# Optimization experiments

Measured on AMD Instinct MI355X. Metric: run time of the kernel, lower is better.

Reference implementation:

```python
import jax, jax.numpy as jnp
import numpy as np

EPS = 1e-5
GROUPS = 8


def _gn_per_channel(x, w, b):
    # GroupNorm with num_groups == num_channels: per-channel instance norm over (h, w)
    m = x.mean(axis=(2, 3), keepdims=True)
    v = x.var(axis=(2, 3), keepdims=True)  # biased var, matches torch GroupNorm
    xn = (x - m) * jax.lax.rsqrt(v + EPS)
    return xn * w[None, :, None, None] + b[None, :, None, None]


def setup_inputs() -> dict:
    key = jax.random.key(0)
    k0, k1 = jax.random.split(key)
    b, c, h, w = 16, 512, 64, 64
    cg = c // GROUPS          # 64 per-group channels
    half = cg // 2            # 32
    x = jax.random.normal(k0, (b, c, h, w), jnp.float32)
    conv1x1_w = jax.random.normal(k1, (cg, cg), jnp.float32) / np.float32(np.sqrt(cg))
    conv1x1_b = jnp.zeros((cg,), jnp.float32)
    gn_w = jnp.ones((cg,), jnp.float32)
    gn_b = jnp.zeros((cg,), jnp.float32)
    gn1_w = jnp.ones((half,), jnp.float32)
    gn1_b = jnp.zeros((half,), jnp.float32)
    cweight = jnp.zeros((1, half, 1, 1), jnp.float32)
    cbias = jnp.ones((1, half, 1, 1), jnp.float32)
    sweight = jnp.zeros((1, half, 1, 1), jnp.float32)
    sbias = jnp.ones((1, half, 1, 1), jnp.float32)
    return {"x": x, "conv1x1_w": conv1x1_w, "conv1x1_b": conv1x1_b,
            "gn_w": gn_w, "gn_b": gn_b, "gn1_w": gn1_w, "gn1_b": gn1_b,
            "cweight": cweight, "cbias": cbias, "sweight": sweight, "sbias": sbias}


def reference(x, conv1x1_w, conv1x1_b, gn_w, gn_b, gn1_w, gn1_b,
              cweight, cbias, sweight, sbias):
    b, c, h, w = x.shape
    g = GROUPS
    cg = c // g
    half = cg // 2
    bg = b * g
    gx = x.reshape(bg, cg, h, w)  # group_x

    # coordinate-attention branch: pool along W and H
    x_h = gx.mean(axis=3, keepdims=True)                      # (bg, cg, h, 1)
    x_w = gx.mean(axis=2, keepdims=True).transpose(0, 1, 3, 2)  # (bg, cg, w, 1)
    hw_cat = jnp.concatenate([x_h, x_w], axis=2)              # (bg, cg, h+w, 1)
    hw = jnp.einsum('oi,bilk->bolk', conv1x1_w, hw_cat) + conv1x1_b[None, :, None, None]
    xh = hw[:, :, :h]                       # (bg, cg, h, 1)
    xw = hw[:, :, h:].transpose(0, 1, 3, 2)  # (bg, cg, 1, w)
    x1 = _gn_per_channel(gx * jax.nn.sigmoid(xh) * jax.nn.sigmoid(xw), gn_w, gn_b)

    # shuffle-attention branch on chunked channels
    x0, x1b = gx[:, :half], gx[:, half:]
    xc = x0.mean(axis=(2, 3), keepdims=True)                  # (bg, half, 1, 1)
    x_channel = x0 * jax.nn.sigmoid(cweight * xc + cbias)
    xs = _gn_per_channel(x1b, gn1_w, gn1_b)
    x_spatial = x1b * jax.nn.sigmoid(sweight * xs + sbias)
    out = jnp.concatenate([x_channel, x_spatial], axis=1)     # (bg, cg, h, w)
    # channel shuffle with g=2
    x2 = out.reshape(bg, 2, half, h, w).transpose(0, 2, 1, 3, 4).reshape(bg, cg, h, w)

    # cross-branch attention weights via small batched matmuls
    x11 = jax.nn.softmax(x1.mean(axis=(2, 3)).reshape(bg, 1, cg), axis=-1)
    x21 = jax.nn.softmax(x2.mean(axis=(2, 3)).reshape(bg, 1, cg), axis=-1)
    x12 = x2.reshape(bg, cg, h * w)
    x22 = x1.reshape(bg, cg, h * w)
    weights = (jnp.matmul(x11, x12) + jnp.matmul(x21, x22)).reshape(bg, 1, h, w)
    return (gx * jax.nn.sigmoid(weights)).reshape(b, c, h, w)
```

## Files before the change

kernel.cpp:

```cpp
#include <hip/hip_runtime.h>
#include <math.h>

#define EPSV 1e-5f

__device__ __forceinline__ float fast_rcp(float x) {
#if __has_builtin(__builtin_amdgcn_rcpf)
    return __builtin_amdgcn_rcpf(x);
#else
    return 1.0f / x;
#endif
}

__device__ __forceinline__ float sigmoidf_(float x) {
    return fast_rcp(1.0f + __expf(-x));
}

__global__ __launch_bounds__(256) void k_stats1(
    const float* __restrict__ x,
    float* __restrict__ rowmean,
    float* __restrict__ colmean,
    float* __restrict__ meanA,
    float* __restrict__ varA)
{
    int blk = blockIdx.x;
    const float4* p4 = (const float4*)(x + (size_t)blk * 4096);
    int t = threadIdx.x;
    int g = t >> 4, cl = t & 15;
    float cp0 = 0.f, cp1 = 0.f, cp2 = 0.f, cp3 = 0.f, s = 0.f, ss = 0.f;
    __shared__ float colacc[16][64];
    __shared__ float red[8];
#pragma unroll
    for (int k = 0; k < 4; ++k) {
        float4 v = p4[t + 256 * k];
        float rp = v.x + v.y + v.z + v.w;
        s += rp;
        ss += v.x * v.x + v.y * v.y + v.z * v.z + v.w * v.w;
        cp0 += v.x; cp1 += v.y; cp2 += v.z; cp3 += v.w;
#pragma unroll
        for (int m = 8; m >= 1; m >>= 1) rp += __shfl_xor(rp, m, 16);
        if (cl == 0) rowmean[(size_t)blk * 64 + g + 16 * k] = rp * (1.0f / 64.0f);
    }
    colacc[g][cl * 4 + 0] = cp0;
    colacc[g][cl * 4 + 1] = cp1;
    colacc[g][cl * 4 + 2] = cp2;
    colacc[g][cl * 4 + 3] = cp3;
#pragma unroll
    for (int m = 32; m >= 1; m >>= 1) { s += __shfl_xor(s, m); ss += __shfl_xor(ss, m); }
    int wv = t >> 6;
    if ((t & 63) == 0) { red[wv] = s; red[4 + wv] = ss; }
    __syncthreads();
    if (t < 64) {
        float cs = 0.f;
#pragma unroll
        for (int gg = 0; gg < 16; ++gg) cs += colacc[gg][t];
        colmean[(size_t)blk * 64 + t] = cs * (1.0f / 64.0f);
    }
    if (t == 0) {
        float S = red[0] + red[1] + red[2] + red[3];
        float SS = red[4] + red[5] + red[6] + red[7];
        float m = S * (1.0f / 4096.0f);
        meanA[blk] = m;
        varA[blk] = SS * (1.0f / 4096.0f) - m * m;
    }
}

__global__ __launch_bounds__(256) void k_conv(
    const float* __restrict__ W, const float* __restrict__ Wb,
    const float* __restrict__ rowmean, const float* __restrict__ colmean,
    float* __restrict__ shg, float* __restrict__ swg)
{
    int blk = blockIdx.x;
    int bg = blk >> 1, rc = blk & 1;
    const float* rm = (rc ? colmean : rowmean) + (size_t)bg * 4096;
    float* outp = (rc ? swg : shg) + (size_t)bg * 4096;
    int t = threadIdx.x, lane = t & 63, wv = t >> 6;
    float r[64];
#pragma unroll
    for (int i = 0; i < 64; ++i) r[i] = rm[i * 64 + lane];
    for (int j = 0; j < 16; ++j) {
        int c = wv * 16 + j;
        float acc = Wb[c];
#pragma unroll
        for (int i = 0; i < 64; ++i)
            acc = fmaf(W[c * 64 + i], r[i], acc);
        outp[c * 64 + lane] = sigmoidf_(acc);
    }
}

__global__ __launch_bounds__(256) void k_stats2(
    const float* __restrict__ x,
    const float* __restrict__ shg, const float* __restrict__ swg,
    const float* __restrict__ meanA, const float* __restrict__ varA,
    const float* __restrict__ swt, const float* __restrict__ sbs,
    const float* __restrict__ gn1w, const float* __restrict__ gn1b,
    float* __restrict__ meanT, float* __restrict__ varT,
    float* __restrict__ spat)
{
    int blk = blockIdx.x;
    int c = blk & 63, bg = blk >> 6;
    const float4* p4 = (const float4*)(x + (size_t)blk * 4096);
    int t = threadIdx.x;
    int g = t >> 4, cl = t & 15;
    float4 sw4 = ((const float4*)(swg + (size_t)blk * 64))[cl];
    float a = 0.f, bb = 0.f;
    bool spatial = (c >= 32);
    if (spatial) {
        int i = c - 32;
        float mu = meanA[blk];
        float r2 = rsqrtf(varA[blk] + EPSV);
        a = swt[i] * gn1w[i] * r2;
        bb = swt[i] * (gn1b[i] - mu * r2 * gn1w[i]) + sbs[i];
    }
    float st = 0.f, sst = 0.f, ssp = 0.f;
#pragma unroll
    for (int k = 0; k < 4; ++k) {
        float4 v = p4[t + 256 * k];
        float sh = shg[(size_t)blk * 64 + g + 16 * k];
        float t0 = v.x * sh * sw4.x;
        float t1 = v.y * sh * sw4.y;
        float t2 = v.z * sh * sw4.z;
        float t3 = v.w * sh * sw4.w;
        st += t0 + t1 + t2 + t3;
        sst += t0 * t0 + t1 * t1 + t2 * t2 + t3 * t3;
        if (spatial) {
            ssp += v.x * sigmoidf_(fmaf(a, v.x, bb))
                 + v.y * sigmoidf_(fmaf(a, v.y, bb))
                 + v.z * sigmoidf_(fmaf(a, v.z, bb))
                 + v.w * sigmoidf_(fmaf(a, v.w, bb));
        }
    }
#pragma unroll
    for (int m = 32; m >= 1; m >>= 1) {
        st += __shfl_xor(st, m); sst += __shfl_xor(sst, m); ssp += __shfl_xor(ssp, m);
    }
    __shared__ float red[12];
    int wv = t >> 6;
    if ((t & 63) == 0) { red[wv] = st; red[4 + wv] = sst; red[8 + wv] = ssp; }
    __syncthreads();
    if (t == 0) {
        float S = red[0] + red[1] + red[2] + red[3];
        float SS = red[4] + red[5] + red[6] + red[7];
        float m = S * (1.0f / 4096.0f);
        meanT[blk] = m;
        varT[blk] = SS * (1.0f / 4096.0f) - m * m;
        if (spatial) {
            float SP = red[8] + red[9] + red[10] + red[11];
            spat[bg * 32 + (c - 32)] = SP * (1.0f / 4096.0f);
        }
    }
}

__global__ __launch_bounds__(64) void k_coef(
    const float* __restrict__ meanA, const float* __restrict__ varA,
    const float* __restrict__ meanT, const float* __restrict__ varT,
    const float* __restrict__ spat,
    const float* __restrict__ gnw, const float* __restrict__ gnb,
    const float* __restrict__ gn1w, const float* __restrict__ gn1b,
    const float* __restrict__ cwt, const float* __restrict__ cbs,
    const float* __restrict__ swt, const float* __restrict__ sbs,
    float* __restrict__ eArr,
    float* __restrict__ gArr,
    float* __restrict__ dArr,
    float* __restrict__ aArr,
    float* __restrict__ bArr,
    float* __restrict__ kArr)
{
    int bg = blockIdx.x;
    int c = threadIdx.x;
    size_t idx = (size_t)bg * 64 + c;
    __shared__ float x2m[64], x11L[64], sL[32];
    if (c < 32) {
        float xc = meanA[idx];
        float s = sigmoidf_(fmaf(cwt[c], xc, cbs[c]));
        sL[c] = s;
        x2m[2 * c] = s * xc;
        x2m[2 * c + 1] = spat[bg * 32 + c];
    }
    __syncthreads();
    float v1 = gnb[c];
    float mx = v1;
#pragma unroll
    for (int m = 32; m >= 1; m >>= 1) mx = fmaxf(mx, __shfl_xor(mx, m));
    float e1 = __expf(v1 - mx);
    float s1 = e1;
#pragma unroll
    for (int m = 32; m >= 1; m >>= 1) s1 += __shfl_xor(s1, m);
    float x11 = e1 / s1;
    x11L[c] = x11;
    float v2 = x2m[c];
    mx = v2;
#pragma unroll
    for (int m = 32; m >= 1; m >>= 1) mx = fmaxf(mx, __shfl_xor(mx, m));
    float e2 = __expf(v2 - mx);
    float s2 = e2;
#pragma unroll
    for (int m = 32; m >= 1; m >>= 1) s2 += __shfl_xor(s2, m);
    float x21 = e2 / s2;

    float mt = meanT[idx];
    float rt = rsqrtf(varT[idx] + EPSV);
    eArr[idx] = x21 * gnw[c] * rt;
    float kp = x21 * (gnb[c] - gnw[c] * rt * mt);
#pragma unroll
    for (int m = 32; m >= 1; m >>= 1) kp += __shfl_xor(kp, m);
    if (c == 0) kArr[bg] = kp;
    __syncthreads();
    if (c < 32) {
        gArr[bg * 32 + c] = x11L[2 * c] * sL[c];
        dArr[bg * 32 + c] = x11L[2 * c + 1];
        size_t idx2 = (size_t)bg * 64 + 32 + c;
        float mu = meanA[idx2];
        float r2 = rsqrtf(varA[idx2] + EPSV);
        aArr[bg * 32 + c] = swt[c] * gn1w[c] * r2;
        bArr[bg * 32 + c] = swt[c] * (gn1b[c] - mu * r2 * gn1w[c]) + sbs[c];
    }
}

__global__ __launch_bounds__(256) void k_final(
    const float* __restrict__ x,
    const float* __restrict__ shg, const float* __restrict__ swg,
    const float* __restrict__ eArr, const float* __restrict__ gArr,
    const float* __restrict__ dArr, const float* __restrict__ aArr,
    const float* __restrict__ bArr, const float* __restrict__ kArr,
    float* __restrict__ outp)
{
    int blk = blockIdx.x;
    int bg = blk >> 2, tile = blk & 3;
    int h0 = tile << 4;
    int t = threadIdx.x;
    __shared__ float shL[64][16];
    __shared__ float4 swL[64][16];
    __shared__ float eL[64], gL[32], dL[32], aL[32], bL[32];
    for (int idx = t; idx < 1024; idx += 256) {
        int c = idx >> 4, q = idx & 15;
        shL[c][q] = shg[((size_t)bg * 64 + c) * 64 + h0 + q];
        swL[c][q] = ((const float4*)swg)[((size_t)bg * 64 + c) * 16 + q];
    }
    if (t < 64)       eL[t]        = eArr[(size_t)bg * 64 + t];
    else if (t < 96)  gL[t - 64]   = gArr[bg * 32 + t - 64];
    else if (t < 128) dL[t - 96]   = dArr[bg * 32 + t - 96];
    else if (t < 160) aL[t - 128]  = aArr[bg * 32 + t - 128];
    else if (t < 192) bL[t - 160]  = bArr[bg * 32 + t - 160];
    __syncthreads();
    int hl = t >> 4, w4 = t & 15;
    const float* xp = x + (size_t)bg * 64 * 4096 + (size_t)(h0 + hl) * 64 + w4 * 4;
    float K = kArr[bg];
    float ax = K, ay = K, az = K, aw = K;
#pragma unroll 8
    for (int c = 0; c < 32; ++c) {
        float4 v = *(const float4*)(xp + (size_t)c * 4096);
        float4 s4 = swL[c][w4];
        float ce = eL[c] * shL[c][hl];
        float gc = gL[c];
        ax = fmaf(fmaf(ce, s4.x, gc), v.x, ax);
        ay = fmaf(fmaf(ce, s4.y, gc), v.y, ay);
        az = fmaf(fmaf(ce, s4.z, gc), v.z, az);
        aw = fmaf(fmaf(ce, s4.w, gc), v.w, aw);
    }
#pragma unroll 8
    for (int i = 0; i < 32; ++i) {
        int c = 32 + i;
        float4 v = *(const float4*)(xp + (size_t)c * 4096);
        float4 s4 = swL[c][w4];
        float ce = eL[c] * shL[c][hl];
        float ai = aL[i], bi = bL[i], di = dL[i];
        ax = fmaf(ce * s4.x, v.x, ax); ax = fmaf(di * v.x, sigmoidf_(fmaf(ai, v.x, bi)), ax);
        ay = fmaf(ce * s4.y, v.y, ay); ay = fmaf(di * v.y, sigmoidf_(fmaf(ai, v.y, bi)), ay);
        az = fmaf(ce * s4.z, v.z, az); az = fmaf(di * v.z, sigmoidf_(fmaf(ai, v.z, bi)), az);
        aw = fmaf(ce * s4.w, v.w, aw); aw = fmaf(di * v.w, sigmoidf_(fmaf(ai, v.w, bi)), aw);
    }
    float sx = sigmoidf_(ax), sy = sigmoidf_(ay), sz = sigmoidf_(az), sw_ = sigmoidf_(aw);
    float* op = outp + (xp - x);
#pragma unroll 8
    for (int c = 0; c < 64; ++c) {
        float4 v = *(const float4*)(xp + (size_t)c * 4096);
        float4 o = { v.x * sx, v.y * sy, v.z * sz, v.w * sw_ };
        *(float4*)(op + (size_t)c * 4096) = o;
    }
}

extern "C" void kernel_launch(void* const* d_in, const int* in_sizes, int n_in,
                              void* d_out, int out_size, void* d_ws, size_t ws_size,
                              hipStream_t stream) {
    (void)in_sizes; (void)n_in; (void)out_size; (void)ws_size;
    const float* x    = (const float*)d_in[0];
    const float* W    = (const float*)d_in[1];
    const float* Wb   = (const float*)d_in[2];
    const float* gnw  = (const float*)d_in[3];
    const float* gnb  = (const float*)d_in[4];
    const float* gn1w = (const float*)d_in[5];
    const float* gn1b = (const float*)d_in[6];
    const float* cwt  = (const float*)d_in[7];
    const float* cbs  = (const float*)d_in[8];
    const float* swt  = (const float*)d_in[9];
    const float* sbs  = (const float*)d_in[10];
    float* out = (float*)d_out;
    float* ws = (float*)d_ws;

    float* rowmean = ws;
    float* colmean = rowmean + 524288;
    float* shg     = colmean + 524288;
    float* swg     = shg + 524288;
    float* meanA   = swg + 524288;
    float* varA    = meanA + 8192;
    float* meanT   = varA + 8192;
    float* varT    = meanT + 8192;
    float* spat    = varT + 8192;
    float* eArr    = spat + 4096;
    float* gArr    = eArr + 8192;
    float* dArr    = gArr + 4096;
    float* aArr    = dArr + 4096;
    float* bArr    = aArr + 4096;
    float* kArr    = bArr + 4096;

    k_stats1<<<8192, 256, 0, stream>>>(x, rowmean, colmean, meanA, varA);
    k_conv<<<256, 256, 0, stream>>>(W, Wb, rowmean, colmean, shg, swg);
    k_stats2<<<8192, 256, 0, stream>>>(x, shg, swg, meanA, varA, swt, sbs, gn1w, gn1b,
                                       meanT, varT, spat);
    k_coef<<<128, 64, 0, stream>>>(meanA, varA, meanT, varT, spat, gnw, gnb, gn1w, gn1b,
                                   cwt, cbs, swt, sbs, eArr, gArr, dArr, aArr, bArr, kArr);
    k_final<<<512, 256, 0, stream>>>(x, shg, swg, eArr, gArr, dArr, aArr, bArr, kArr, out);
}
```

Baseline: 349.7 us.

## Merge five kernels into one cooperative persistent kernel with grid syncs

Replaces the five separate launches with a single templated persistent kernel that runs all phases under cooperative launch, separated by grid-wide syncs. A separate multi-launch path remains as a fallback. The statistics passes now give each wavefront one plane instead of one block per plane, so the per-block shared-memory column reduction becomes shuffles. The final pass uses 8-row bands with float2 accesses and caches the whole swg tile in LDS. The aim is to remove launch gaps and tail effects between phases. In exchange, the fused kernel is limited to the blocks that can be resident at once, and the grid syncs and host-side attribute and occupancy queries on every call add cost.

```diff
diff --git a/kernel.cpp b/kernel.cpp
--- a/kernel.cpp
+++ b/kernel.cpp
@@ -1,5 +1,8 @@
 #include <hip/hip_runtime.h>
+#include <hip/hip_cooperative_groups.h>
 #include <math.h>
+
+namespace cg = cooperative_groups;
 
 #define EPSV 1e-5f
 
@@ -15,267 +18,266 @@
     return fast_rcp(1.0f + __expf(-x));
 }
 
-__global__ __launch_bounds__(256) void k_stats1(
+union SharedU {
+    struct { float x2m[64]; float x11L[64]; float sL[32]; } d;
+    struct {
+        float swf[64 * 64];
+        float shf[64 * 8];
+        float eL[64];
+        float gL[32], dL[32], aL[32], bL[32];
+    } e;
+};
+
+template<int PHASE>
+__global__ __launch_bounds__(256, 2) void mega(
     const float* __restrict__ x,
-    float* __restrict__ rowmean,
-    float* __restrict__ colmean,
-    float* __restrict__ meanA,
-    float* __restrict__ varA)
-{
-    int blk = blockIdx.x;
-    const float4* p4 = (const float4*)(x + (size_t)blk * 4096);
-    int t = threadIdx.x;
-    int g = t >> 4, cl = t & 15;
-    float cp0 = 0.f, cp1 = 0.f, cp2 = 0.f, cp3 = 0.f, s = 0.f, ss = 0.f;
-    __shared__ float colacc[16][64];
-    __shared__ float red[8];
-#pragma unroll
-    for (int k = 0; k < 4; ++k) {
-        float4 v = p4[t + 256 * k];
-        float rp = v.x + v.y + v.z + v.w;
-        s += rp;
-        ss += v.x * v.x + v.y * v.y + v.z * v.z + v.w * v.w;
-        cp0 += v.x; cp1 += v.y; cp2 += v.z; cp3 += v.w;
-#pragma unroll
-        for (int m = 8; m >= 1; m >>= 1) rp += __shfl_xor(rp, m, 16);
-        if (cl == 0) rowmean[(size_t)blk * 64 + g + 16 * k] = rp * (1.0f / 64.0f);
-    }
-    colacc[g][cl * 4 + 0] = cp0;
-    colacc[g][cl * 4 + 1] = cp1;
-    colacc[g][cl * 4 + 2] = cp2;
-    colacc[g][cl * 4 + 3] = cp3;
-#pragma unroll
-    for (int m = 32; m >= 1; m >>= 1) { s += __shfl_xor(s, m); ss += __shfl_xor(ss, m); }
-    int wv = t >> 6;
-    if ((t & 63) == 0) { red[wv] = s; red[4 + wv] = ss; }
-    __syncthreads();
-    if (t < 64) {
-        float cs = 0.f;
-#pragma unroll
-        for (int gg = 0; gg < 16; ++gg) cs += colacc[gg][t];
-        colmean[(size_t)blk * 64 + t] = cs * (1.0f / 64.0f);
-    }
-    if (t == 0) {
-        float S = red[0] + red[1] + red[2] + red[3];
-        float SS = red[4] + red[5] + red[6] + red[7];
-        float m = S * (1.0f / 4096.0f);
-        meanA[blk] = m;
-        varA[blk] = SS * (1.0f / 4096.0f) - m * m;
-    }
-}
-
-__global__ __launch_bounds__(256) void k_conv(
     const float* __restrict__ W, const float* __restrict__ Wb,
-    const float* __restrict__ rowmean, const float* __restrict__ colmean,
-    float* __restrict__ shg, float* __restrict__ swg)
-{
-    int blk = blockIdx.x;
-    int bg = blk >> 1, rc = blk & 1;
-    const float* rm = (rc ? colmean : rowmean) + (size_t)bg * 4096;
-    float* outp = (rc ? swg : shg) + (size_t)bg * 4096;
-    int t = threadIdx.x, lane = t & 63, wv = t >> 6;
-    float r[64];
-#pragma unroll
-    for (int i = 0; i < 64; ++i) r[i] = rm[i * 64 + lane];
-    for (int j = 0; j < 16; ++j) {
-        int c = wv * 16 + j;
-        float acc = Wb[c];
-#pragma unroll
-        for (int i = 0; i < 64; ++i)
-            acc = fmaf(W[c * 64 + i], r[i], acc);
-        outp[c * 64 + lane] = sigmoidf_(acc);
-    }
-}
-
-__global__ __launch_bounds__(256) void k_stats2(
-    const float* __restrict__ x,
-    const float* __restrict__ shg, const float* __restrict__ swg,
-    const float* __restrict__ meanA, const float* __restrict__ varA,
-    const float* __restrict__ swt, const float* __restrict__ sbs,
-    const float* __restrict__ gn1w, const float* __restrict__ gn1b,
-    float* __restrict__ meanT, float* __restrict__ varT,
-    float* __restrict__ spat)
-{
-    int blk = blockIdx.x;
-    int c = blk & 63, bg = blk >> 6;
-    const float4* p4 = (const float4*)(x + (size_t)blk * 4096);
-    int t = threadIdx.x;
-    int g = t >> 4, cl = t & 15;
-    float4 sw4 = ((const float4*)(swg + (size_t)blk * 64))[cl];
-    float a = 0.f, bb = 0.f;
-    bool spatial = (c >= 32);
-    if (spatial) {
-        int i = c - 32;
-        float mu = meanA[blk];
-        float r2 = rsqrtf(varA[blk] + EPSV);
-        a = swt[i] * gn1w[i] * r2;
-        bb = swt[i] * (gn1b[i] - mu * r2 * gn1w[i]) + sbs[i];
-    }
-    float st = 0.f, sst = 0.f, ssp = 0.f;
-#pragma unroll
-    for (int k = 0; k < 4; ++k) {
-        float4 v = p4[t + 256 * k];
-        float sh = shg[(size_t)blk * 64 + g + 16 * k];
-        float t0 = v.x * sh * sw4.x;
-        float t1 = v.y * sh * sw4.y;
-        float t2 = v.z * sh * sw4.z;
-        float t3 = v.w * sh * sw4.w;
-        st += t0 + t1 + t2 + t3;
-        sst += t0 * t0 + t1 * t1 + t2 * t2 + t3 * t3;
-        if (spatial) {
-            ssp += v.x * sigmoidf_(fmaf(a, v.x, bb))
-                 + v.y * sigmoidf_(fmaf(a, v.y, bb))
-                 + v.z * sigmoidf_(fmaf(a, v.z, bb))
-                 + v.w * sigmoidf_(fmaf(a, v.w, bb));
-        }
-    }
-#pragma unroll
-    for (int m = 32; m >= 1; m >>= 1) {
-        st += __shfl_xor(st, m); sst += __shfl_xor(sst, m); ssp += __shfl_xor(ssp, m);
-    }
-    __shared__ float red[12];
-    int wv = t >> 6;
-    if ((t & 63) == 0) { red[wv] = st; red[4 + wv] = sst; red[8 + wv] = ssp; }
-    __syncthreads();
-    if (t == 0) {
-        float S = red[0] + red[1] + red[2] + red[3];
-        float SS = red[4] + red[5] + red[6] + red[7];
-        float m = S * (1.0f / 4096.0f);
-        meanT[blk] = m;
-        varT[blk] = SS * (1.0f / 4096.0f) - m * m;
-        if (spatial) {
-            float SP = red[8] + red[9] + red[10] + red[11];
-            spat[bg * 32 + (c - 32)] = SP * (1.0f / 4096.0f);
-        }
-    }
-}
-
-__global__ __launch_bounds__(64) void k_coef(
-    const float* __restrict__ meanA, const float* __restrict__ varA,
-    const float* __restrict__ meanT, const float* __restrict__ varT,
-    const float* __restrict__ spat,
     const float* __restrict__ gnw, const float* __restrict__ gnb,
     const float* __restrict__ gn1w, const float* __restrict__ gn1b,
     const float* __restrict__ cwt, const float* __restrict__ cbs,
     const float* __restrict__ swt, const float* __restrict__ sbs,
-    float* __restrict__ eArr,
-    float* __restrict__ gArr,
-    float* __restrict__ dArr,
-    float* __restrict__ aArr,
-    float* __restrict__ bArr,
-    float* __restrict__ kArr)
+    float* __restrict__ out, float* __restrict__ ws)
 {
-    int bg = blockIdx.x;
-    int c = threadIdx.x;
-    size_t idx = (size_t)bg * 64 + c;
-    __shared__ float x2m[64], x11L[64], sL[32];
-    if (c < 32) {
-        float xc = meanA[idx];
-        float s = sigmoidf_(fmaf(cwt[c], xc, cbs[c]));
-        sL[c] = s;
-        x2m[2 * c] = s * xc;
-        x2m[2 * c + 1] = spat[bg * 32 + c];
-    }
-    __syncthreads();
-    float v1 = gnb[c];
-    float mx = v1;
-#pragma unroll
-    for (int m = 32; m >= 1; m >>= 1) mx = fmaxf(mx, __shfl_xor(mx, m));
-    float e1 = __expf(v1 - mx);
-    float s1 = e1;
-#pragma unroll
-    for (int m = 32; m >= 1; m >>= 1) s1 += __shfl_xor(s1, m);
-    float x11 = e1 / s1;
-    x11L[c] = x11;
-    float v2 = x2m[c];
-    mx = v2;
-#pragma unroll
-    for (int m = 32; m >= 1; m >>= 1) mx = fmaxf(mx, __shfl_xor(mx, m));
-    float e2 = __expf(v2 - mx);
-    float s2 = e2;
-#pragma unroll
-    for (int m = 32; m >= 1; m >>= 1) s2 += __shfl_xor(s2, m);
-    float x21 = e2 / s2;
-
-    float mt = meanT[idx];
-    float rt = rsqrtf(varT[idx] + EPSV);
-    eArr[idx] = x21 * gnw[c] * rt;
-    float kp = x21 * (gnb[c] - gnw[c] * rt * mt);
-#pragma unroll
-    for (int m = 32; m >= 1; m >>= 1) kp += __shfl_xor(kp, m);
-    if (c == 0) kArr[bg] = kp;
-    __syncthreads();
-    if (c < 32) {
-        gArr[bg * 32 + c] = x11L[2 * c] * sL[c];
-        dArr[bg * 32 + c] = x11L[2 * c + 1];
-        size_t idx2 = (size_t)bg * 64 + 32 + c;
-        float mu = meanA[idx2];
-        float r2 = rsqrtf(varA[idx2] + EPSV);
-        aArr[bg * 32 + c] = swt[c] * gn1w[c] * r2;
-        bArr[bg * 32 + c] = swt[c] * (gn1b[c] - mu * r2 * gn1w[c]) + sbs[c];
-    }
-}
-
-__global__ __launch_bounds__(256) void k_final(
-    const float* __restrict__ x,
-    const float* __restrict__ shg, const float* __restrict__ swg,
-    const float* __restrict__ eArr, const float* __restrict__ gArr,
-    const float* __restrict__ dArr, const float* __restrict__ aArr,
-    const float* __restrict__ bArr, const float* __restrict__ kArr,
-    float* __restrict__ outp)
-{
-    int blk = blockIdx.x;
-    int bg = blk >> 2, tile = blk & 3;
-    int h0 = tile << 4;
-    int t = threadIdx.x;
-    __shared__ float shL[64][16];
-    __shared__ float4 swL[64][16];
-    __shared__ float eL[64], gL[32], dL[32], aL[32], bL[32];
-    for (int idx = t; idx < 1024; idx += 256) {
-        int c = idx >> 4, q = idx & 15;
-        shL[c][q] = shg[((size_t)bg * 64 + c) * 64 + h0 + q];
-        swL[c][q] = ((const float4*)swg)[((size_t)bg * 64 + c) * 16 + q];
-    }
-    if (t < 64)       eL[t]        = eArr[(size_t)bg * 64 + t];
-    else if (t < 96)  gL[t - 64]   = gArr[bg * 32 + t - 64];
-    else if (t < 128) dL[t - 96]   = dArr[bg * 32 + t - 96];
-    else if (t < 160) aL[t - 128]  = aArr[bg * 32 + t - 128];
-    else if (t < 192) bL[t - 160]  = bArr[bg * 32 + t - 160];
-    __syncthreads();
-    int hl = t >> 4, w4 = t & 15;
-    const float* xp = x + (size_t)bg * 64 * 4096 + (size_t)(h0 + hl) * 64 + w4 * 4;
-    float K = kArr[bg];
-    float ax = K, ay = K, az = K, aw = K;
+    __shared__ SharedU sm;
+
+    float* rowmean = ws;
+    float* colmean = rowmean + 524288;
+    float* shg     = colmean + 524288;
+    float* swg     = shg + 524288;
+    float* meanA   = swg + 524288;
+    float* varA    = meanA + 8192;
+    float* meanT   = varA + 8192;
+    float* varT    = meanT + 8192;
+    float* spat    = varT + 8192;
+    float* eArr    = spat + 4096;
+    float* gArr    = eArr + 8192;
+    float* dArr    = gArr + 4096;
+    float* aArr    = dArr + 4096;
+    float* bArr    = aArr + 4096;
+    float* kArr    = bArr + 4096;
+
+    const int t = threadIdx.x;
+    const int l = t & 63;
+    const int wv = t >> 6;
+    const int stride = gridDim.x;
+
+    if (PHASE < 0 || PHASE == 0) {
+      for (int u = blockIdx.x; u < 2048; u += stride) {
+        int plane = u * 4 + wv;
+        const float4* p4 = (const float4*)(x + (size_t)plane * 4096);
+        float c0 = 0.f, c1 = 0.f, c2 = 0.f, c3 = 0.f, s = 0.f, ss = 0.f;
+#pragma unroll 4
+        for (int k = 0; k < 16; ++k) {
+            float4 v = p4[k * 64 + l];
+            float rp = v.x + v.y + v.z + v.w;
+            s += rp;
+            ss += v.x * v.x + v.y * v.y + v.z * v.z + v.w * v.w;
+            c0 += v.x; c1 += v.y; c2 += v.z; c3 += v.w;
+#pragma unroll
+            for (int m = 8; m >= 1; m >>= 1) rp += __shfl_xor(rp, m, 16);
+            if ((l & 15) == 0)
+                rowmean[(size_t)plane * 64 + k * 4 + (l >> 4)] = rp * (1.f / 64.f);
+        }
+#pragma unroll
+        for (int m = 32; m >= 16; m >>= 1) {
+            c0 += __shfl_xor(c0, m); c1 += __shfl_xor(c1, m);
+            c2 += __shfl_xor(c2, m); c3 += __shfl_xor(c3, m);
+        }
+        if (l < 16) {
+            float4 cm = { c0 * (1.f / 64.f), c1 * (1.f / 64.f),
+                          c2 * (1.f / 64.f), c3 * (1.f / 64.f) };
+            ((float4*)(colmean + (size_t)plane * 64))[l] = cm;
+        }
+#pragma unroll
+        for (int m = 32; m >= 1; m >>= 1) { s += __shfl_xor(s, m); ss += __shfl_xor(ss, m); }
+        if (l == 0) {
+            float mn = s * (1.f / 4096.f);
+            meanA[plane] = mn;
+            varA[plane] = ss * (1.f / 4096.f) - mn * mn;
+        }
+      }
+    }
+    if constexpr (PHASE < 0) cg::this_grid().sync();
+
+    if (PHASE < 0 || PHASE == 1) {
+      for (int u = blockIdx.x; u < 256; u += stride) {
+        int bgc = u >> 1, rc = u & 1;
+        const float* rm = (rc ? colmean : rowmean) + (size_t)bgc * 4096;
+        float* outp = (rc ? swg : shg) + (size_t)bgc * 4096;
+        float r[64];
+#pragma unroll
+        for (int i = 0; i < 64; ++i) r[i] = rm[i * 64 + l];
+        for (int jj = 0; jj < 16; ++jj) {
+            int c = wv * 16 + jj;
+            float acc = Wb[c];
+#pragma unroll
+            for (int i = 0; i < 64; ++i) acc = fmaf(W[c * 64 + i], r[i], acc);
+            outp[c * 64 + l] = sigmoidf_(acc);
+        }
+      }
+    }
+    if constexpr (PHASE < 0) cg::this_grid().sync();
+
+    if (PHASE < 0 || PHASE == 2) {
+      for (int u = blockIdx.x; u < 2048; u += stride) {
+        int plane = u * 4 + wv;
+        int cch = plane & 63, bgc = plane >> 6;
+        const float4* p4 = (const float4*)(x + (size_t)plane * 4096);
+        float4 sw4 = ((const float4*)(swg + (size_t)plane * 64))[l & 15];
+        float a = 0.f, bb = 0.f;
+        bool spatial = (cch >= 32);
+        if (spatial) {
+            int i = cch - 32;
+            float mu = meanA[plane];
+            float r2 = rsqrtf(varA[plane] + EPSV);
+            a = swt[i] * gn1w[i] * r2;
+            bb = swt[i] * (gn1b[i] - mu * r2 * gn1w[i]) + sbs[i];
+        }
+        float st = 0.f, sst = 0.f, ssp = 0.f;
+#pragma unroll 4
+        for (int k = 0; k < 16; ++k) {
+            float4 v = p4[k * 64 + l];
+            float sh = shg[(size_t)plane * 64 + k * 4 + (l >> 4)];
+            float t0 = v.x * sh * sw4.x;
+            float t1 = v.y * sh * sw4.y;
+            float t2 = v.z * sh * sw4.z;
+            float t3 = v.w * sh * sw4.w;
+            st += t0 + t1 + t2 + t3;
+            sst += t0 * t0 + t1 * t1 + t2 * t2 + t3 * t3;
+            if (spatial) {
+                ssp += v.x * sigmoidf_(fmaf(a, v.x, bb))
+                     + v.y * sigmoidf_(fmaf(a, v.y, bb))
+                     + v.z * sigmoidf_(fmaf(a, v.z, bb))
+                     + v.w * sigmoidf_(fmaf(a, v.w, bb));
+            }
+        }
+#pragma unroll
+        for (int m = 32; m >= 1; m >>= 1) {
+            st += __shfl_xor(st, m); sst += __shfl_xor(sst, m); ssp += __shfl_xor(ssp, m);
+        }
+        if (l == 0) {
+            float mn = st * (1.f / 4096.f);
+            meanT[plane] = mn;
+            varT[plane] = sst * (1.f / 4096.f) - mn * mn;
+            if (spatial) spat[bgc * 32 + (cch - 32)] = ssp * (1.f / 4096.f);
+        }
+      }
+    }
+    if constexpr (PHASE < 0) cg::this_grid().sync();
+
+    if (PHASE < 0 || PHASE == 3) {
+      for (int u = blockIdx.x; u < 128; u += stride) {
+        int bgc = u;
+        if (t < 32) {
+            size_t idx = (size_t)bgc * 64 + t;
+            float xc = meanA[idx];
+            float s = sigmoidf_(fmaf(cwt[t], xc, cbs[t]));
+            sm.d.sL[t] = s;
+            sm.d.x2m[2 * t] = s * xc;
+            sm.d.x2m[2 * t + 1] = spat[bgc * 32 + t];
+        }
+        __syncthreads();
+        if (t < 64) {
+            int c = t;
+            size_t idx = (size_t)bgc * 64 + c;
+            float v1 = gnb[c];
+            float mx = v1;
+#pragma unroll
+            for (int m = 32; m >= 1; m >>= 1) mx = fmaxf(mx, __shfl_xor(mx, m));
+            float e1 = __expf(v1 - mx);
+            float s1 = e1;
+#pragma unroll
+            for (int m = 32; m >= 1; m >>= 1) s1 += __shfl_xor(s1, m);
+            sm.d.x11L[c] = e1 / s1;
+
+            float v2 = sm.d.x2m[c];
+            mx = v2;
+#pragma unroll
+            for (int m = 32; m >= 1; m >>= 1) mx = fmaxf(mx, __shfl_xor(mx, m));
+            float e2 = __expf(v2 - mx);
+            float s2 = e2;
+#pragma unroll
+            for (int m = 32; m >= 1; m >>= 1) s2 += __shfl_xor(s2, m);
+            float x21 = e2 / s2;
+
+            float mt = meanT[idx];
+            float rt = rsqrtf(varT[idx] + EPSV);
+            eArr[idx] = x21 * gnw[c] * rt;
+            float kp = x21 * (gnb[c] - gnw[c] * rt * mt);
+#pragma unroll
+            for (int m = 32; m >= 1; m >>= 1) kp += __shfl_xor(kp, m);
+            if (c == 0) kArr[bgc] = kp;
+        }
+        __syncthreads();
+        if (t < 32) {
+            gArr[bgc * 32 + t] = sm.d.x11L[2 * t] * sm.d.sL[t];
+            dArr[bgc * 32 + t] = sm.d.x11L[2 * t + 1];
+            size_t idx2 = (size_t)bgc * 64 + 32 + t;
+            float mu = meanA[idx2];
+            float r2 = rsqrtf(varA[idx2] + EPSV);
+            aArr[bgc * 32 + t] = swt[t] * gn1w[t] * r2;
+            bArr[bgc * 32 + t] = swt[t] * (gn1b[t] - mu * r2 * gn1w[t]) + sbs[t];
+        }
+        __syncthreads();
+      }
+    }
+    if constexpr (PHASE < 0) cg::this_grid().sync();
+
+    if (PHASE < 0 || PHASE == 4) {
+      for (int u = blockIdx.x; u < 1024; u += stride) {
+        int bgc = u >> 3, band = u & 7;
+        int h0 = band * 8;
+#pragma unroll
+        for (int j = 0; j < 4; ++j) {
+            int f = t + 256 * j;
+            ((float4*)sm.e.swf)[f] = ((const float4*)swg)[(size_t)bgc * 1024 + f];
+        }
+#pragma unroll
+        for (int j = 0; j < 2; ++j) {
+            int idx = t + 256 * j;
+            int c = idx >> 3, r = idx & 7;
+            sm.e.shf[c * 8 + r] = shg[(size_t)bgc * 4096 + c * 64 + h0 + r];
+        }
+        if (t < 64)       sm.e.eL[t]       = eArr[(size_t)bgc * 64 + t];
+        else if (t < 96)  sm.e.gL[t - 64]  = gArr[bgc * 32 + t - 64];
+        else if (t < 128) sm.e.dL[t - 96]  = dArr[bgc * 32 + t - 96];
+        else if (t < 160) sm.e.aL[t - 128] = aArr[bgc * 32 + t - 128];
+        else if (t < 192) sm.e.bL[t - 160] = bArr[bgc * 32 + t - 160];
+        float K = kArr[bgc];
+        __syncthreads();
+
+        int hl = t >> 5, w2 = t & 31;
+        const float* xp = x + (size_t)bgc * 262144 + (size_t)(h0 + hl) * 64 + w2 * 2;
+        float ax = K, ay = K;
 #pragma unroll 8
-    for (int c = 0; c < 32; ++c) {
-        float4 v = *(const float4*)(xp + (size_t)c * 4096);
-        float4 s4 = swL[c][w4];
-        float ce = eL[c] * shL[c][hl];
-        float gc = gL[c];
-        ax = fmaf(fmaf(ce, s4.x, gc), v.x, ax);
-        ay = fmaf(fmaf(ce, s4.y, gc), v.y, ay);
-        az = fmaf(fmaf(ce, s4.z, gc), v.z, az);
-        aw = fmaf(fmaf(ce, s4.w, gc), v.w, aw);
-    }
+        for (int c = 0; c < 32; ++c) {
+            float2 v = *(const float2*)(xp + (size_t)c * 4096);
+            float ce = sm.e.eL[c] * sm.e.shf[c * 8 + hl];
+            float gc = sm.e.gL[c];
+            ax = fmaf(fmaf(ce, sm.e.swf[c * 64 + 2 * w2], gc), v.x, ax);
+            ay = fmaf(fmaf(ce, sm.e.swf[c * 64 + 2 * w2 + 1], gc), v.y, ay);
+        }
 #pragma unroll 8
-    for (int i = 0; i < 32; ++i) {
-        int c = 32 + i;
-        float4 v = *(const float4*)(xp + (size_t)c * 4096);
-        float4 s4 = swL[c][w4];
-        float ce = eL[c] * shL[c][hl];
-        float ai = aL[i], bi = bL[i], di = dL[i];
-        ax = fmaf(ce * s4.x, v.x, ax); ax = fmaf(di * v.x, sigmoidf_(fmaf(ai, v.x, bi)), ax);
-        ay = fmaf(ce * s4.y, v.y, ay); ay = fmaf(di * v.y, sigmoidf_(fmaf(ai, v.y, bi)), ay);
-        az = fmaf(ce * s4.z, v.z, az); az = fmaf(di * v.z, sigmoidf_(fmaf(ai, v.z, bi)), az);
-        aw = fmaf(ce * s4.w, v.w, aw); aw = fmaf(di * v.w, sigmoidf_(fmaf(ai, v.w, bi)), aw);
-    }
-    float sx = sigmoidf_(ax), sy = sigmoidf_(ay), sz = sigmoidf_(az), sw_ = sigmoidf_(aw);
-    float* op = outp + (xp - x);
+        for (int i = 0; i < 32; ++i) {
+            int c = 32 + i;
+            float2 v = *(const float2*)(xp + (size_t)c * 4096);
+            float ce = sm.e.eL[c] * sm.e.shf[c * 8 + hl];
+            float ai = sm.e.aL[i], bi = sm.e.bL[i], di = sm.e.dL[i];
+            ax = fmaf(ce * sm.e.swf[c * 64 + 2 * w2], v.x, ax);
+            ax = fmaf(di * v.x, sigmoidf_(fmaf(ai, v.x, bi)), ax);
+            ay = fmaf(ce * sm.e.swf[c * 64 + 2 * w2 + 1], v.y, ay);
+            ay = fmaf(di * v.y, sigmoidf_(fmaf(ai, v.y, bi)), ay);
+        }
+        float sx = sigmoidf_(ax), sy = sigmoidf_(ay);
+        float* op = out + (xp - x);
 #pragma unroll 8
-    for (int c = 0; c < 64; ++c) {
-        float4 v = *(const float4*)(xp + (size_t)c * 4096);
-        float4 o = { v.x * sx, v.y * sy, v.z * sz, v.w * sw_ };
-        *(float4*)(op + (size_t)c * 4096) = o;
+        for (int c = 0; c < 64; ++c) {
+            float2 v = *(const float2*)(xp + (size_t)c * 4096);
+            float2 o = { v.x * sx, v.y * sy };
+            *(float2*)(op + (size_t)c * 4096) = o;
+        }
+        __syncthreads();
+      }
     }
 }
 
@@ -297,27 +299,38 @@
     float* out = (float*)d_out;
     float* ws = (float*)d_ws;
 
-    float* rowmean = ws;
-    float* colmean = rowmean + 524288;
-    float* shg     = colmean + 524288;
-    float* swg     = shg + 524288;
-    float* meanA   = swg + 524288;
-    float* varA    = meanA + 8192;
-    float* meanT   = varA + 8192;
-    float* varT    = meanT + 8192;
-    float* spat    = varT + 8192;
-    float* eArr    = spat + 4096;
-    float* gArr    = eArr + 8192;
-    float* dArr    = gArr + 4096;
-    float* aArr    = dArr + 4096;
-    float* bArr    = aArr + 4096;
-    float* kArr    = bArr + 4096;
-
-    k_stats1<<<8192, 256, 0, stream>>>(x, rowmean, colmean, meanA, varA);
-    k_conv<<<256, 256, 0, stream>>>(W, Wb, rowmean, colmean, shg, swg);
-    k_stats2<<<8192, 256, 0, stream>>>(x, shg, swg, meanA, varA, swt, sbs, gn1w, gn1b,
-                                       meanT, varT, spat);
-    k_coef<<<128, 64, 0, stream>>>(meanA, varA, meanT, varT, spat, gnw, gnb, gn1w, gn1b,
-                                   cwt, cbs, swt, sbs, eArr, gArr, dArr, aArr, bArr, kArr);
-    k_final<<<512, 256, 0, stream>>>(x, shg, swg, eArr, gArr, dArr, aArr, bArr, kArr, out);
+    bool launched = false;
+    int dev = 0;
+    hipGetDevice(&dev);
+    int coopAttr = 0, nCU = 0;
+    hipDeviceGetAttribute(&coopAttr, hipDeviceAttributeCooperativeLaunch, dev);
+    hipDeviceGetAttribute(&nCU, hipDeviceAttributeMultiprocessorCount, dev);
+    auto kfn = mega<-1>;
+    int maxb = 0;
+    if (coopAttr && nCU > 0 &&
+        hipOccupancyMaxActiveBlocksPerMultiprocessor(
+            &maxb, reinterpret_cast<const void*>(kfn), 256, 0) == hipSuccess &&
+        maxb > 0) {
+        int nb = maxb * nCU;
+        if (nb > 2048) nb = 2048;
+        void* args[] = { (void*)&x, (void*)&W, (void*)&Wb, (void*)&gnw, (void*)&gnb,
+                         (void*)&gn1w, (void*)&gn1b, (void*)&cwt, (void*)&cbs,
+                         (void*)&swt, (void*)&sbs, (void*)&out, (void*)&ws };
+        if (hipLaunchCooperativeKernel(reinterpret_cast<const void*>(kfn),
+                                       dim3(nb), dim3(256), args, 0, stream)
+            == hipSuccess)
+            launched = true;
+    }
+    if (!launched) {
+        mega<0><<<2048, 256, 0, stream>>>(x, W, Wb, gnw, gnb, gn1w, gn1b,
+                                          cwt, cbs, swt, sbs, out, ws);
+        mega<1><<<256, 256, 0, stream>>>(x, W, Wb, gnw, gnb, gn1w, gn1b,
+                                         cwt, cbs, swt, sbs, out, ws);
+        mega<2><<<2048, 256, 0, stream>>>(x, W, Wb, gnw, gnb, gn1w, gn1b,
+                                          cwt, cbs, swt, sbs, out, ws);
+        mega<3><<<128, 256, 0, stream>>>(x, W, Wb, gnw, gnb, gn1w, gn1b,
+                                         cwt, cbs, swt, sbs, out, ws);
+        mega<4><<<1024, 256, 0, stream>>>(x, W, Wb, gnw, gnb, gn1w, gn1b,
+                                          cwt, cbs, swt, sbs, out, ws);
+    }
 }
```

Measured after the change: 585.0 us. 67.3% more time.

## Map one wavefront per plane in stats kernels; nontemporal stores in final

Applied to the files above, without the earlier changes.

Both stats kernels now assign one 64-lane wavefront to each 4096-element plane, so there are 4 planes per block. This removes the shared-memory reductions and __syncthreads, and the block count drops by a factor of four. Column sums are reduced with cross-lane shuffles instead of an LDS accumulator. The final kernel stages swg with coalesced float4 copies into a flat LDS array and writes the output with nontemporal stores, which spends fewer cache resources on write-only data. Each thread now handles more loads serially, which could lower memory-level parallelism per wave.

```diff
diff --git a/kernel.cpp b/kernel.cpp
--- a/kernel.cpp
+++ b/kernel.cpp
@@ -2,6 +2,8 @@
 #include <math.h>
 
 #define EPSV 1e-5f
+
+typedef float vfloat4 __attribute__((ext_vector_type(4)));
 
 __device__ __forceinline__ float fast_rcp(float x) {
 #if __has_builtin(__builtin_amdgcn_rcpf)
@@ -15,52 +17,45 @@
     return fast_rcp(1.0f + __expf(-x));
 }
 
-__global__ __launch_bounds__(256) void k_stats1(
+__global__ __launch_bounds__(256) void k_statsA(
     const float* __restrict__ x,
     float* __restrict__ rowmean,
     float* __restrict__ colmean,
     float* __restrict__ meanA,
     float* __restrict__ varA)
 {
-    int blk = blockIdx.x;
-    const float4* p4 = (const float4*)(x + (size_t)blk * 4096);
-    int t = threadIdx.x;
-    int g = t >> 4, cl = t & 15;
-    float cp0 = 0.f, cp1 = 0.f, cp2 = 0.f, cp3 = 0.f, s = 0.f, ss = 0.f;
-    __shared__ float colacc[16][64];
-    __shared__ float red[8];
-#pragma unroll
-    for (int k = 0; k < 4; ++k) {
-        float4 v = p4[t + 256 * k];
+    const int t = threadIdx.x, l = t & 63, wv = t >> 6;
+    const int plane = blockIdx.x * 4 + wv;
+    const float4* p4 = (const float4*)(x + (size_t)plane * 4096);
+    float c0 = 0.f, c1 = 0.f, c2 = 0.f, c3 = 0.f, s = 0.f, ss = 0.f;
+#pragma unroll 8
+    for (int k = 0; k < 16; ++k) {
+        float4 v = p4[k * 64 + l];
         float rp = v.x + v.y + v.z + v.w;
         s += rp;
         ss += v.x * v.x + v.y * v.y + v.z * v.z + v.w * v.w;
-        cp0 += v.x; cp1 += v.y; cp2 += v.z; cp3 += v.w;
+        c0 += v.x; c1 += v.y; c2 += v.z; c3 += v.w;
 #pragma unroll
         for (int m = 8; m >= 1; m >>= 1) rp += __shfl_xor(rp, m, 16);
-        if (cl == 0) rowmean[(size_t)blk * 64 + g + 16 * k] = rp * (1.0f / 64.0f);
-    }
-    colacc[g][cl * 4 + 0] = cp0;
-    colacc[g][cl * 4 + 1] = cp1;
-    colacc[g][cl * 4 + 2] = cp2;
-    colacc[g][cl * 4 + 3] = cp3;
+        if ((l & 15) == 0)
+            rowmean[(size_t)plane * 64 + k * 4 + (l >> 4)] = rp * (1.f / 64.f);
+    }
+#pragma unroll
+    for (int m = 32; m >= 16; m >>= 1) {
+        c0 += __shfl_xor(c0, m); c1 += __shfl_xor(c1, m);
+        c2 += __shfl_xor(c2, m); c3 += __shfl_xor(c3, m);
+    }
+    if (l < 16) {
+        float4 cm = { c0 * (1.f / 64.f), c1 * (1.f / 64.f),
+                      c2 * (1.f / 64.f), c3 * (1.f / 64.f) };
+        ((float4*)(colmean + (size_t)plane * 64))[l] = cm;
+    }
 #pragma unroll
     for (int m = 32; m >= 1; m >>= 1) { s += __shfl_xor(s, m); ss += __shfl_xor(ss, m); }
-    int wv = t >> 6;
-    if ((t & 63) == 0) { red[wv] = s; red[4 + wv] = ss; }
-    __syncthreads();
-    if (t < 64) {
-        float cs = 0.f;
-#pragma unroll
-        for (int gg = 0; gg < 16; ++gg) cs += colacc[gg][t];
-        colmean[(size_t)blk * 64 + t] = cs * (1.0f / 64.0f);
-    }
-    if (t == 0) {
-        float S = red[0] + red[1] + red[2] + red[3];
-        float SS = red[4] + red[5] + red[6] + red[7];
-        float m = S * (1.0f / 4096.0f);
-        meanA[blk] = m;
-        varA[blk] = SS * (1.0f / 4096.0f) - m * m;
+    if (l == 0) {
+        float mn = s * (1.f / 4096.f);
+        meanA[plane] = mn;
+        varA[plane] = ss * (1.f / 4096.f) - mn * mn;
     }
 }
 
@@ -87,7 +82,7 @@
     }
 }
 
-__global__ __launch_bounds__(256) void k_stats2(
+__global__ __launch_bounds__(256) void k_statsC(
     const float* __restrict__ x,
     const float* __restrict__ shg, const float* __restrict__ swg,
     const float* __restrict__ meanA, const float* __restrict__ varA,
@@ -96,26 +91,25 @@
     float* __restrict__ meanT, float* __restrict__ varT,
     float* __restrict__ spat)
 {
-    int blk = blockIdx.x;
-    int c = blk & 63, bg = blk >> 6;
-    const float4* p4 = (const float4*)(x + (size_t)blk * 4096);
-    int t = threadIdx.x;
-    int g = t >> 4, cl = t & 15;
-    float4 sw4 = ((const float4*)(swg + (size_t)blk * 64))[cl];
+    const int t = threadIdx.x, l = t & 63, wv = t >> 6;
+    const int plane = blockIdx.x * 4 + wv;
+    const int cch = plane & 63, bgc = plane >> 6;
+    const float4* p4 = (const float4*)(x + (size_t)plane * 4096);
+    float4 sw4 = ((const float4*)(swg + (size_t)plane * 64))[l & 15];
     float a = 0.f, bb = 0.f;
-    bool spatial = (c >= 32);
+    const bool spatial = (cch >= 32);
     if (spatial) {
-        int i = c - 32;
-        float mu = meanA[blk];
-        float r2 = rsqrtf(varA[blk] + EPSV);
+        int i = cch - 32;
+        float mu = meanA[plane];
+        float r2 = rsqrtf(varA[plane] + EPSV);
         a = swt[i] * gn1w[i] * r2;
         bb = swt[i] * (gn1b[i] - mu * r2 * gn1w[i]) + sbs[i];
     }
     float st = 0.f, sst = 0.f, ssp = 0.f;
-#pragma unroll
-    for (int k = 0; k < 4; ++k) {
-        float4 v = p4[t + 256 * k];
-        float sh = shg[(size_t)blk * 64 + g + 16 * k];
+#pragma unroll 8
+    for (int k = 0; k < 16; ++k) {
+        float4 v = p4[k * 64 + l];
+        float sh = shg[(size_t)plane * 64 + k * 4 + (l >> 4)];
         float t0 = v.x * sh * sw4.x;
         float t1 = v.y * sh * sw4.y;
         float t2 = v.z * sh * sw4.z;
@@ -133,20 +127,11 @@
     for (int m = 32; m >= 1; m >>= 1) {
         st += __shfl_xor(st, m); sst += __shfl_xor(sst, m); ssp += __shfl_xor(ssp, m);
     }
-    __shared__ float red[12];
-    int wv = t >> 6;
-    if ((t & 63) == 0) { red[wv] = st; red[4 + wv] = sst; red[8 + wv] = ssp; }
-    __syncthreads();
-    if (t == 0) {
-        float S = red[0] + red[1] + red[2] + red[3];
-        float SS = red[4] + red[5] + red[6] + red[7];
-        float m = S * (1.0f / 4096.0f);
-        meanT[blk] = m;
-        varT[blk] = SS * (1.0f / 4096.0f) - m * m;
-        if (spatial) {
-            float SP = red[8] + red[9] + red[10] + red[11];
-            spat[bg * 32 + (c - 32)] = SP * (1.0f / 4096.0f);
-        }
+    if (l == 0) {
+        float mn = st * (1.f / 4096.f);
+        meanT[plane] = mn;
+        varT[plane] = sst * (1.f / 4096.f) - mn * mn;
+        if (spatial) spat[bgc * 32 + (cch - 32)] = ssp * (1.f / 4096.f);
     }
 }
 
@@ -158,12 +143,9 @@
     const float* __restrict__ gn1w, const float* __restrict__ gn1b,
     const float* __restrict__ cwt, const float* __restrict__ cbs,
     const float* __restrict__ swt, const float* __restrict__ sbs,
-    float* __restrict__ eArr,
-    float* __restrict__ gArr,
-    float* __restrict__ dArr,
-    float* __restrict__ aArr,
-    float* __restrict__ bArr,
-    float* __restrict__ kArr)
+    float* __restrict__ eArr, float* __restrict__ gArr,
+    float* __restrict__ dArr, float* __restrict__ aArr,
+    float* __restrict__ bArr, float* __restrict__ kArr)
 {
     int bg = blockIdx.x;
     int c = threadIdx.x;
@@ -224,58 +206,66 @@
     const float* __restrict__ bArr, const float* __restrict__ kArr,
     float* __restrict__ outp)
 {
-    int blk = blockIdx.x;
-    int bg = blk >> 2, tile = blk & 3;
-    int h0 = tile << 4;
-    int t = threadIdx.x;
-    __shared__ float shL[64][16];
-    __shared__ float4 swL[64][16];
+    const int blk = blockIdx.x;
+    const int bg = blk >> 2, tile = blk & 3;
+    const int h0 = tile << 4;
+    const int t = threadIdx.x;
+    __shared__ float swf[64 * 64];
+    __shared__ float shf[64 * 16];
     __shared__ float eL[64], gL[32], dL[32], aL[32], bL[32];
-    for (int idx = t; idx < 1024; idx += 256) {
-        int c = idx >> 4, q = idx & 15;
-        shL[c][q] = shg[((size_t)bg * 64 + c) * 64 + h0 + q];
-        swL[c][q] = ((const float4*)swg)[((size_t)bg * 64 + c) * 16 + q];
-    }
-    if (t < 64)       eL[t]        = eArr[(size_t)bg * 64 + t];
-    else if (t < 96)  gL[t - 64]   = gArr[bg * 32 + t - 64];
-    else if (t < 128) dL[t - 96]   = dArr[bg * 32 + t - 96];
-    else if (t < 160) aL[t - 128]  = aArr[bg * 32 + t - 128];
-    else if (t < 192) bL[t - 160]  = bArr[bg * 32 + t - 160];
+#pragma unroll
+    for (int j = 0; j < 4; ++j) {
+        int f = t + 256 * j;
+        ((float4*)swf)[f] = ((const float4*)swg)[(size_t)bg * 1024 + f];
+    }
+#pragma unroll
+    for (int j = 0; j < 4; ++j) {
+        int idx = t + 256 * j;
+        int c = idx >> 4, r = idx & 15;
+        shf[idx] = shg[(size_t)bg * 4096 + c * 64 + h0 + r];
+    }
+    if (t < 64)       eL[t]       = eArr[(size_t)bg * 64 + t];
+    else if (t < 96)  gL[t - 64]  = gArr[bg * 32 + t - 64];
+    else if (t < 128) dL[t - 96]  = dArr[bg * 32 + t - 96];
+    else if (t < 160) aL[t - 128] = aArr[bg * 32 + t - 128];
+    else if (t < 192) bL[t - 160] = bArr[bg * 32 + t - 160];
+    const float K = kArr[bg];
     __syncthreads();
-    int hl = t >> 4, w4 = t & 15;
-    const float* xp = x + (size_t)bg * 64 * 4096 + (size_t)(h0 + hl) * 64 + w4 * 4;
-    float K = kArr[bg];
+
+    const int hl = t >> 4, w4 = t & 15;
+    const float* xp = x + (size_t)bg * 262144 + (size_t)(h0 + hl) * 64 + w4 * 4;
     float ax = K, ay = K, az = K, aw = K;
 #pragma unroll 8
     for (int c = 0; c < 32; ++c) {
         float4 v = *(const float4*)(xp + (size_t)c * 4096);
-        float4 s4 = swL[c][w4];
-        float ce = eL[c] * shL[c][hl];
+        float ce = eL[c] * shf[c * 16 + hl];
         float gc = gL[c];
-        ax = fmaf(fmaf(ce, s4.x, gc), v.x, ax);
-        ay = fmaf(fmaf(ce, s4.y, gc), v.y, ay);
-        az = fmaf(fmaf(ce, s4.z, gc), v.z, az);
-        aw = fmaf(fmaf(ce, s4.w, gc), v.w, aw);
+        const float* swc = &swf[c * 64 + w4 * 4];
+        ax = fmaf(fmaf(ce, swc[0], gc), v.x, ax);
+        ay = fmaf(fmaf(ce, swc[1], gc), v.y, ay);
+        az = fmaf(fmaf(ce, swc[2], gc), v.z, az);
+        aw = fmaf(fmaf(ce, swc[3], gc), v.w, aw);
     }
 #pragma unroll 8
     for (int i = 0; i < 32; ++i) {
         int c = 32 + i;
         float4 v = *(const float4*)(xp + (size_t)c * 4096);
-        float4 s4 = swL[c][w4];
-        float ce = eL[c] * shL[c][hl];
+        float ce = eL[c] * shf[c * 16 + hl];
         float ai = aL[i], bi = bL[i], di = dL[i];
-        ax = fmaf(ce * s4.x, v.x, ax); ax = fmaf(di * v.x, sigmoidf_(fmaf(ai, v.x, bi)), ax);
-        ay = fmaf(ce * s4.y, v.y, ay); ay = fmaf(di * v.y, sigmoidf_(fmaf(ai, v.y, bi)), ay);
-        az = fmaf(ce * s4.z, v.z, az); az = fmaf(di * v.z, sigmoidf_(fmaf(ai, v.z, bi)), az);
-        aw = fmaf(ce * s4.w, v.w, aw); aw = fmaf(di * v.w, sigmoidf_(fmaf(ai, v.w, bi)), aw);
-    }
-    float sx = sigmoidf_(ax), sy = sigmoidf_(ay), sz = sigmoidf_(az), sw_ = sigmoidf_(aw);
+        const float* swc = &swf[c * 64 + w4 * 4];
+        ax = fmaf(ce * swc[0], v.x, ax); ax = fmaf(di * v.x, sigmoidf_(fmaf(ai, v.x, bi)), ax);
+        ay = fmaf(ce * swc[1], v.y, ay); ay = fmaf(di * v.y, sigmoidf_(fmaf(ai, v.y, bi)), ay);
+        az = fmaf(ce * swc[2], v.z, az); az = fmaf(di * v.z, sigmoidf_(fmaf(ai, v.z, bi)), az);
+        aw = fmaf(ce * swc[3], v.w, aw); aw = fmaf(di * v.w, sigmoidf_(fmaf(ai, v.w, bi)), aw);
+    }
+    const float sx = sigmoidf_(ax), sy = sigmoidf_(ay),
+                sz = sigmoidf_(az), sw_ = sigmoidf_(aw);
     float* op = outp + (xp - x);
 #pragma unroll 8
     for (int c = 0; c < 64; ++c) {
         float4 v = *(const float4*)(xp + (size_t)c * 4096);
-        float4 o = { v.x * sx, v.y * sy, v.z * sz, v.w * sw_ };
-        *(float4*)(op + (size_t)c * 4096) = o;
+        vfloat4 o = { v.x * sx, v.y * sy, v.z * sz, v.w * sw_ };
+        __builtin_nontemporal_store(o, (vfloat4*)(op + (size_t)c * 4096));
     }
 }
 
@@ -313,9 +303,9 @@
     float* bArr    = aArr + 4096;
     float* kArr    = bArr + 4096;
 
-    k_stats1<<<8192, 256, 0, stream>>>(x, rowmean, colmean, meanA, varA);
+    k_statsA<<<2048, 256, 0, stream>>>(x, rowmean, colmean, meanA, varA);
     k_conv<<<256, 256, 0, stream>>>(W, Wb, rowmean, colmean, shg, swg);
-    k_stats2<<<8192, 256, 0, stream>>>(x, shg, swg, meanA, varA, swt, sbs, gn1w, gn1b,
+    k_statsC<<<2048, 256, 0, stream>>>(x, shg, swg, meanA, varA, swt, sbs, gn1w, gn1b,
                                        meanT, varT, spat);
     k_coef<<<128, 64, 0, stream>>>(meanA, varA, meanT, varT, spat, gnw, gnb, gn1w, gn1b,
                                    cwt, cbs, swt, sbs, eArr, gArr, dArr, aArr, bArr, kArr);
```

Result: faster. 340.8 us (-2.6%).
